# Kernel optimization log

Measured on AMD Instinct MI355X. Metric: run time of the kernel, lower is better.

The kernel has to match this reference:

```python
import jax, jax.numpy as jnp
import numpy as np

# GDN (gated delta-rule) linear attention, prefill path, single packed sequence,
# no initial conv/ssm state.
NUM_K_HEADS = 16
NUM_V_HEADS = 32
HEAD_K_DIM = 128
HEAD_V_DIM = 128
HIDDEN = 2048
CONV_K = 4
EPS = 1e-6
K_TOTAL = NUM_K_HEADS * HEAD_K_DIM
V_TOTAL = NUM_V_HEADS * HEAD_V_DIM
QKV_TOTAL = 2 * K_TOTAL + V_TOTAL


def setup_inputs() -> dict:
    key = jax.random.key(0)
    ks = jax.random.split(key, 9)
    T = 2048
    s = 0.02
    return {
        "hidden_states": jax.random.normal(ks[0], (T, HIDDEN), jnp.float32),
        "in_proj_qkv_weight": s * jax.random.normal(ks[1], (QKV_TOTAL, HIDDEN), jnp.float32),
        "in_proj_z_weight": s * jax.random.normal(ks[2], (V_TOTAL, HIDDEN), jnp.float32),
        "in_proj_a_weight": s * jax.random.normal(ks[3], (NUM_V_HEADS, HIDDEN), jnp.float32),
        "in_proj_b_weight": s * jax.random.normal(ks[4], (NUM_V_HEADS, HIDDEN), jnp.float32),
        "conv1d_weight": 0.1 * jax.random.normal(ks[5], (QKV_TOTAL, CONV_K), jnp.float32),
        "out_proj_weight": s * jax.random.normal(ks[6], (HIDDEN, V_TOTAL), jnp.float32),
        "norm_weight": jnp.ones((HEAD_V_DIM,), jnp.float32),
        "A_log": jnp.log(jnp.linspace(1.0, 8.0, NUM_V_HEADS, dtype=jnp.float32)),
        "dt_bias": 0.5 * jax.random.normal(ks[7], (NUM_V_HEADS,), jnp.float32),
    }


def _causal_conv1d_silu(x, w):
    # x: [T, C], w: [C, K] depthwise causal conv + SiLU
    T = x.shape[0]
    K = w.shape[1]
    xp = jnp.pad(x, ((K - 1, 0), (0, 0)))
    y = xp[0:T] * w[:, 0]
    for j in range(1, K):  # small fixed K
        y = y + xp[j:j + T] * w[:, j]
    return jax.nn.silu(y)


def _l2norm(x):
    return x / jnp.sqrt(jnp.sum(x * x, axis=-1, keepdims=True) + EPS)


def _gdn_recurrence(q, k, v, g, beta, scale):
    # q,k: [T,Hv,Dk] (l2-normed, repeated over GQA groups), v: [T,Hv,Dv]
    # g,beta: [T,Hv]. State S: [Hv,Dk,Dv]. Gated delta rule:
    #   S <- exp(g)*S ; S <- S + k^T beta (v - k S) ; o = scale * q S
    Hv, Dk = q.shape[1], q.shape[2]
    Dv = v.shape[2]

    def step(S, inp):
        q_t, k_t, v_t, g_t, b_t = inp
        S = S * jnp.exp(g_t)[:, None, None]
        pred = jnp.einsum('hk,hkv->hv', k_t, S)
        delta = b_t[:, None] * (v_t - pred)
        S = S + jnp.einsum('hk,hv->hkv', k_t, delta)
        o = jnp.einsum('hk,hkv->hv', q_t * scale, S)
        return S, o

    S0 = jnp.zeros((Hv, Dk, Dv), q.dtype)
    _, o = jax.lax.scan(step, S0, (q, k, v, g, beta))
    return o  # [T,Hv,Dv]


def reference(hidden_states, in_proj_qkv_weight, in_proj_z_weight, in_proj_a_weight,
              in_proj_b_weight, conv1d_weight, out_proj_weight, norm_weight, A_log, dt_bias):
    T = hidden_states.shape[0]
    mixed = hidden_states @ in_proj_qkv_weight.T            # [T, QKV_TOTAL]
    z = hidden_states @ in_proj_z_weight.T                  # [T, V_TOTAL]
    a = hidden_states @ in_proj_a_weight.T                  # [T, Hv]
    b = hidden_states @ in_proj_b_weight.T                  # [T, Hv]

    mixed = _causal_conv1d_silu(mixed, conv1d_weight)

    q, k, v = jnp.split(mixed, [K_TOTAL, 2 * K_TOTAL], axis=-1)
    q = q.reshape(T, NUM_K_HEADS, HEAD_K_DIM)
    k = k.reshape(T, NUM_K_HEADS, HEAD_K_DIM)
    v = v.reshape(T, NUM_V_HEADS, HEAD_V_DIM)

    # qk l2-norm in kernel, GQA repeat to v heads
    q = _l2norm(q)
    k = _l2norm(k)
    ratio = NUM_V_HEADS // NUM_K_HEADS
    q = jnp.repeat(q, ratio, axis=1)
    k = jnp.repeat(k, ratio, axis=1)

    # fused_gdn_gating: g = -exp(A_log) * softplus(a + dt_bias); beta = sigmoid(b)
    g = -jnp.exp(A_log) * jax.nn.softplus(a + dt_bias)      # [T,Hv]
    beta = jax.nn.sigmoid(b)                                # [T,Hv]

    o = _gdn_recurrence(q, k, v, g, beta, HEAD_K_DIM ** -0.5)  # [T,Hv,Dv]

    # gated RMSNorm: rmsnorm(o) * norm_weight * silu(z)
    o = o * jax.lax.rsqrt(jnp.mean(o * o, axis=-1, keepdims=True) + EPS) * norm_weight
    o = o * jax.nn.silu(z.reshape(T, NUM_V_HEADS, HEAD_V_DIM))

    return o.reshape(T, -1) @ out_proj_weight.T             # [T, HIDDEN]
```

## Files before the change

### kernel.cpp

```cpp
#include <hip/hip_runtime.h>
#include <math.h>

#define T_SEQ     2048
#define HIDDEN_D  2048
#define NUM_KH    16
#define NUM_VH    32
#define HEAD_DIM  128
#define K_TOTAL   2048
#define V_TOTAL   4096
#define QKV_TOTAL 8192
#define EPS_F     1e-6f
#define CC        32
#define NCHUNK    (T_SEQ / CC)
#define NV        8

typedef __attribute__((ext_vector_type(4))) float f32x4;
typedef __attribute__((ext_vector_type(8))) short s16x8;

__device__ __forceinline__ unsigned short f2bf(float f) {
    unsigned int u = __float_as_uint(f);
    u += 0x7FFFu + ((u >> 16) & 1u);
    return (unsigned short)(u >> 16);
}

__device__ __forceinline__ float bf2f(unsigned short h) {
    return __uint_as_float((unsigned int)h << 16);
}

__global__ __launch_bounds__(256) void cast_bf16_kernel(
    const float* __restrict__ src, unsigned short* __restrict__ dst, int n4)
{
    int idx = blockIdx.x * 256 + threadIdx.x;
    if (idx >= n4) return;
    float4 v = ((const float4*)src)[idx];
    ushort4 o;
    o.x = f2bf(v.x); o.y = f2bf(v.y); o.z = f2bf(v.z); o.w = f2bf(v.w);
    ((ushort4*)dst)[idx] = o;
}

__global__ __launch_bounds__(256) void gemm_bt_bf16(
    const unsigned short* __restrict__ A, const unsigned short* __restrict__ B,
    float* __restrict__ C, int M, int N, int K)
{
    __shared__ unsigned short As[128 * 64];
    __shared__ unsigned short Bs[128 * 64];
    const int tid  = threadIdx.x;
    const int wave = tid >> 6;
    const int lane = tid & 63;
    const int m0 = blockIdx.y * 128;
    const int n0 = blockIdx.x * 128;
    const int wm = (wave >> 1) * 64;
    const int wn = (wave & 1) * 64;

    f32x4 acc[4][4];
    f32x4 zero = {0.f, 0.f, 0.f, 0.f};
#pragma unroll
    for (int i = 0; i < 4; ++i)
#pragma unroll
        for (int j = 0; j < 4; ++j) acc[i][j] = zero;

    const int srow = lane >> 3;
    const int scol = (lane & 7) * 8;
    const int rm = lane & 15;
    const int koq = (lane >> 4) * 8;

    for (int kt = 0; kt < K; kt += 64) {
#pragma unroll
        for (int l = 0; l < 4; ++l) {
            const int r0 = wave * 32 + l * 8;
            const unsigned short* ga =
                A + (size_t)(m0 + r0 + srow) * K + kt + scol;
            const unsigned short* gb =
                B + (size_t)(n0 + r0 + srow) * K + kt + scol;
            __builtin_amdgcn_global_load_lds(
                (const __attribute__((address_space(1))) void*)ga,
                (__attribute__((address_space(3))) void*)&As[r0 * 64], 16, 0, 0);
            __builtin_amdgcn_global_load_lds(
                (const __attribute__((address_space(1))) void*)gb,
                (__attribute__((address_space(3))) void*)&Bs[r0 * 64], 16, 0, 0);
        }
        __syncthreads();

#pragma unroll
        for (int ks = 0; ks < 2; ++ks) {
            const int ko = ks * 32 + koq;
            s16x8 af[4], bfr[4];
#pragma unroll
            for (int i = 0; i < 4; ++i) {
                af[i]  = *(const s16x8*)&As[(wm + i * 16 + rm) * 64 + ko];
                bfr[i] = *(const s16x8*)&Bs[(wn + i * 16 + rm) * 64 + ko];
            }
#pragma unroll
            for (int i = 0; i < 4; ++i)
#pragma unroll
                for (int j = 0; j < 4; ++j)
                    acc[i][j] = __builtin_amdgcn_mfma_f32_16x16x32_bf16(
                        af[i], bfr[j], acc[i][j], 0, 0, 0);
        }
        __syncthreads();
    }

    const int cr = (lane >> 4) * 4;
    const int ccol = lane & 15;
#pragma unroll
    for (int i = 0; i < 4; ++i)
#pragma unroll
        for (int j = 0; j < 4; ++j) {
#pragma unroll
            for (int r = 0; r < 4; ++r)
                C[(size_t)(m0 + wm + i * 16 + cr + r) * N
                  + n0 + wn + j * 16 + ccol] = acc[i][j][r];
        }
}

__global__ __launch_bounds__(256) void gemm_nt_64(
    const float* __restrict__ A, const float* __restrict__ B,
    float* __restrict__ C, int M, int N, int K)
{
    __shared__ float As[16][68];
    __shared__ float Bs[16][68];
    const int tid = threadIdx.x;
    const int m0 = blockIdx.y * 64;
    const int n0 = blockIdx.x * 64;
    const int tm = tid >> 4;
    const int tn = tid & 15;
    const int lr = tid >> 2;
    const int lc = (tid & 3) * 4;

    float acc[4][4];
#pragma unroll
    for (int i = 0; i < 4; ++i)
#pragma unroll
        for (int j = 0; j < 4; ++j) acc[i][j] = 0.f;

    for (int kt = 0; kt < K; kt += 16) {
        float4 av = *(const float4*)(A + (size_t)(m0 + lr) * K + kt + lc);
        float4 bv = *(const float4*)(B + (size_t)(n0 + lr) * K + kt + lc);
        As[lc + 0][lr] = av.x; As[lc + 1][lr] = av.y;
        As[lc + 2][lr] = av.z; As[lc + 3][lr] = av.w;
        Bs[lc + 0][lr] = bv.x; Bs[lc + 1][lr] = bv.y;
        Bs[lc + 2][lr] = bv.z; Bs[lc + 3][lr] = bv.w;
        __syncthreads();
#pragma unroll
        for (int kk = 0; kk < 16; ++kk) {
            float4 a4 = *(const float4*)&As[kk][tm * 4];
            float4 b4 = *(const float4*)&Bs[kk][tn * 4];
            float a[4] = {a4.x, a4.y, a4.z, a4.w};
            float b[4] = {b4.x, b4.y, b4.z, b4.w};
#pragma unroll
            for (int i = 0; i < 4; ++i)
#pragma unroll
                for (int j = 0; j < 4; ++j)
                    acc[i][j] = fmaf(a[i], b[j], acc[i][j]);
        }
        __syncthreads();
    }
#pragma unroll
    for (int i = 0; i < 4; ++i) {
        float4 o = make_float4(acc[i][0], acc[i][1], acc[i][2], acc[i][3]);
        *(float4*)(C + (size_t)(m0 + tm * 4 + i) * N + n0 + tn * 4) = o;
    }
}

__global__ __launch_bounds__(256) void concat_ab_kernel(
    const float* __restrict__ Wa, const float* __restrict__ Wb,
    float* __restrict__ Wab)
{
    int idx = blockIdx.x * 256 + threadIdx.x;
    int half = 16384;
    const float* src = (idx < half) ? Wa : Wb;
    int off = (idx < half) ? idx : idx - half;
    ((float4*)Wab)[idx] = ((const float4*)src)[off];
}

__global__ __launch_bounds__(256) void gating_finalize_kernel(
    const float* __restrict__ ab, const float* __restrict__ A_log,
    const float* __restrict__ dt_bias, float* __restrict__ g,
    float* __restrict__ beta)
{
    int idx = blockIdx.x * 256 + threadIdx.x;
    int t = idx >> 5, h = idx & 31;
    float a = ab[t * 64 + h] + dt_bias[h];
    float b = ab[t * 64 + 32 + h];
    float sp = (a > 20.f) ? a : log1pf(expf(a));
    g[idx] = -expf(A_log[h]) * sp;
    beta[idx] = 1.f / (1.f + expf(-b));
}

__global__ __launch_bounds__(256) void conv_silu_kernel(
    const float* __restrict__ mixed, const float* __restrict__ cw,
    float* __restrict__ qkv)
{
    int idx = blockIdx.x * 256 + threadIdx.x;
    int c = idx & (QKV_TOTAL - 1);
    int t = idx >> 13;
    const float4 w = *(const float4*)(cw + (size_t)c * 4);
    float y = w.w * mixed[(size_t)t * QKV_TOTAL + c];
    if (t >= 1) y = fmaf(w.z, mixed[(size_t)(t - 1) * QKV_TOTAL + c], y);
    if (t >= 2) y = fmaf(w.y, mixed[(size_t)(t - 2) * QKV_TOTAL + c], y);
    if (t >= 3) y = fmaf(w.x, mixed[(size_t)(t - 3) * QKV_TOTAL + c], y);
    qkv[(size_t)t * QKV_TOTAL + c] = y / (1.f + expf(-y));
}

__global__ __launch_bounds__(64) void l2norm_kernel(float* __restrict__ qkv)
{
    const int row = blockIdx.x;
    const int t = row >> 5;
    const int r = row & 31;
    float* p = qkv + (size_t)t * QKV_TOTAL + r * HEAD_DIM;
    const int lane = threadIdx.x;
    float2 v = *(float2*)(p + lane * 2);
    float s = v.x * v.x + v.y * v.y;
    for (int off = 32; off > 0; off >>= 1) s += __shfl_down(s, off);
    s = __shfl(s, 0);
    float inv = rsqrtf(s + EPS_F);
    v.x *= inv; v.y *= inv;
    *(float2*)(p + lane * 2) = v;
}

__global__ __launch_bounds__(256) void gdn_p1(
    const float* __restrict__ qkv, const float* __restrict__ g,
    const float* __restrict__ beta, float* __restrict__ PTbuf,
    unsigned short* __restrict__ K2buf, float* __restrict__ lam_g,
    float* __restrict__ bet_g)
{
    __shared__ float Kn[CC][132];
    __shared__ float Qn[CC][132];
    __shared__ float Wm[CC][33];
    __shared__ float Tld[CC][36];
    __shared__ float Pm[CC][33];
    __shared__ float Trl[CC][33];
    __shared__ float cums[CC];
    __shared__ float betas[CC];
    __shared__ float rlS[CC];

    const int tid = threadIdx.x;
    const int h   = blockIdx.x;
    const int cix = blockIdx.y;
    const int t0  = cix * CC;
    const int kh  = h >> 1;
    const float scale = 0.08838834764831845f;
    const size_t mb = ((size_t)cix * NUM_VH + h);
    const size_t sb = mb * CC;

    if (tid < CC) {
        float x = g[(size_t)(t0 + tid) * NUM_VH + h];
        float bv = beta[(size_t)(t0 + tid) * NUM_VH + h];
#pragma unroll
        for (int off = 1; off < 32; off <<= 1) {
            float n = __shfl_up(x, off);
            if (tid >= off) x += n;
        }
        cums[tid] = x;
        betas[tid] = bv;
        float c31 = __shfl(x, 31);
        lam_g[sb + tid] = expf(x);
        bet_g[sb + tid] = bv;
        rlS[tid] = expf(c31 - x);
    }
#pragma unroll
    for (int p = 0; p < 4; ++p) {
        int idx = p * 256 + tid;
        int i = idx >> 5, k4 = (idx & 31) * 4;
        const float* qr = qkv + (size_t)(t0 + i) * QKV_TOTAL + kh * HEAD_DIM + k4;
        float4 q4 = *(const float4*)qr;
        float4 k4v = *(const float4*)(qr + K_TOTAL);
        *(float4*)&Kn[i][k4] = k4v;
        q4.x *= scale; q4.y *= scale; q4.z *= scale; q4.w *= scale;
        *(float4*)&Qn[i][k4] = q4;
    }
    __syncthreads();

    {
        const int i0 = (tid >> 4) * 2, j0 = (tid & 15) * 2;
        float wa[2][2] = {{0.f, 0.f}, {0.f, 0.f}};
        float pa[2][2] = {{0.f, 0.f}, {0.f, 0.f}};
        for (int k = 0; k < HEAD_DIM; k += 4) {
            float4 a0 = *(const float4*)&Kn[i0][k];
            float4 a1 = *(const float4*)&Kn[i0 + 1][k];
            float4 b0 = *(const float4*)&Kn[j0][k];
            float4 b1 = *(const float4*)&Kn[j0 + 1][k];
            float4 c0 = *(const float4*)&Qn[i0][k];
            float4 c1 = *(const float4*)&Qn[i0 + 1][k];
            const float* ap0 = (const float*)&a0;
            const float* ap1 = (const float*)&a1;
            const float* bp0 = (const float*)&b0;
            const float* bp1 = (const float*)&b1;
            const float* cp0 = (const float*)&c0;
            const float* cp1 = (const float*)&c1;
#pragma unroll
            for (int cc = 0; cc < 4; ++cc) {
                wa[0][0] = fmaf(ap0[cc], bp0[cc], wa[0][0]);
                wa[0][1] = fmaf(ap0[cc], bp1[cc], wa[0][1]);
                wa[1][0] = fmaf(ap1[cc], bp0[cc], wa[1][0]);
                wa[1][1] = fmaf(ap1[cc], bp1[cc], wa[1][1]);
                pa[0][0] = fmaf(cp0[cc], bp0[cc], pa[0][0]);
                pa[0][1] = fmaf(cp0[cc], bp1[cc], pa[0][1]);
                pa[1][0] = fmaf(cp1[cc], bp0[cc], pa[1][0]);
                pa[1][1] = fmaf(cp1[cc], bp1[cc], pa[1][1]);
            }
        }
#pragma unroll
        for (int di = 0; di < 2; ++di)
#pragma unroll
            for (int dj = 0; dj < 2; ++dj) {
                int i = i0 + di, j = j0 + dj;
                float rr = expf(fminf(cums[i] - cums[j], 0.f));
                Wm[i][j] = (j < i) ? betas[i] * rr * wa[di][dj] : 0.f;
                Pm[i][j] = (j <= i) ? rr * pa[di][dj] : 0.f;
            }
    }
    __syncthreads();

    {
        const int col = tid >> 3, tk = tid & 7;
        if (tk == 0) Tld[0][col] = (col == 0) ? 1.f : 0.f;
        for (int i = 1; i < CC; ++i) {
            float part = 0.f;
            for (int j = tk; j < i; j += 8)
                part = fmaf(Wm[i][j], Tld[j][col], part);
            part += __shfl_xor(part, 4);
            part += __shfl_xor(part, 2);
            part += __shfl_xor(part, 1);
            if (tk == 0) Tld[i][col] = ((i == col) ? 1.f : 0.f) - part;
        }
    }
    __syncthreads();

    {
        const int i = tid >> 3, j0 = (tid & 7) * 4;
        const float r = rlS[i];
#pragma unroll
        for (int e = 0; e < 4; ++e)
            Trl[i][j0 + e] = Tld[i][j0 + e] * r;
        float4 accp = {0.f, 0.f, 0.f, 0.f};
        for (int m = 0; m < CC; ++m) {
            float pv = Pm[i][m];
            float4 tv = *(const float4*)&Tld[m][j0];
            accp.x = fmaf(pv, tv.x, accp.x);
            accp.y = fmaf(pv, tv.y, accp.y);
            accp.z = fmaf(pv, tv.z, accp.z);
            accp.w = fmaf(pv, tv.w, accp.w);
        }
        *(float4*)(PTbuf + mb * (CC * CC) + tid * 4) = accp;
    }
    __syncthreads();

    {
        const int m0 = tid >> 3;
        const int q  = (tid & 7) * 4;
        float acc[4][4];
#pragma unroll
        for (int c = 0; c < 4; ++c)
#pragma unroll
            for (int e = 0; e < 4; ++e) acc[c][e] = 0.f;
        for (int j = 0; j < CC; ++j) {
            float t = Trl[j][m0];
#pragma unroll
            for (int c = 0; c < 4; ++c) {
                float4 a = *(const float4*)&Kn[j][q + 32 * c];
                acc[c][0] = fmaf(t, a.x, acc[c][0]);
                acc[c][1] = fmaf(t, a.y, acc[c][1]);
                acc[c][2] = fmaf(t, a.z, acc[c][2]);
                acc[c][3] = fmaf(t, a.w, acc[c][3]);
            }
        }
        unsigned short* kout =
            K2buf + mb * (CC * HEAD_DIM) + m0 * HEAD_DIM + q;
#pragma unroll
        for (int c = 0; c < 4; ++c) {
            ushort4 o4;
            o4.x = f2bf(acc[c][0]); o4.y = f2bf(acc[c][1]);
            o4.z = f2bf(acc[c][2]); o4.w = f2bf(acc[c][3]);
            *(ushort4*)(kout + 32 * c) = o4;
        }
    }
}

__global__ __launch_bounds__(256) void gdn_p2(
    const float* __restrict__ qkv, const float* __restrict__ PTbuf,
    const unsigned short* __restrict__ K2buf, const float* __restrict__ lam_g,
    const float* __restrict__ bet_g, float* __restrict__ o)
{
    __shared__ float Kn[CC][128];
    __shared__ float Qn[CC][128];
    __shared__ unsigned short K2l[2][CC][128];
    __shared__ float PTl[2][CC][36];
    __shared__ float Sm[HEAD_DIM][NV + 2];
    __shared__ float Dl[CC][NV + 2];
    __shared__ float lamS[2][CC], betS[2][CC];

    const int tid = threadIdx.x;
    const int wv  = tid >> 6;
    const int ln  = tid & 63;
    const int h   = blockIdx.x >> 4;
    const int V0  = (blockIdx.x & 15) * NV;
    const int kh  = h >> 1;
    const float scale = 0.08838834764831845f;

    const int ri = tid >> 3;
    const int rn = (tid & 3) * 2;
    const int hh = (tid >> 2) & 1;
    const int hh4 = hh * 4;
    const int rx = ri & 3;

    const int fk = (tid >> 3) * 4;
    const int sn = tid & 7;

    const int drow = wv * 2 + (ln >> 5);
    const int dw   = ln & 31;

#define DMA_KQ(T0)                                                            \
    {                                                                         \
        _Pragma("unroll")                                                     \
        for (int p = 0; p < 4; ++p) {                                         \
            const int i = p * 8 + drow;                                       \
            const int u = dw ^ ((i & 3) << 1);                                \
            const float* sq = qkv + (size_t)((T0) + i) * QKV_TOTAL            \
                              + kh * HEAD_DIM + u * 4;                        \
            __builtin_amdgcn_global_load_lds(                                 \
                (const __attribute__((address_space(1))) void*)(sq + K_TOTAL),\
                (__attribute__((address_space(3))) void*)                     \
                    &Kn[p * 8 + wv * 2][0], 16, 0, 0);                        \
            __builtin_amdgcn_global_load_lds(                                 \
                (const __attribute__((address_space(1))) void*)sq,            \
                (__attribute__((address_space(3))) void*)                     \
                    &Qn[p * 8 + wv * 2][0], 16, 0, 0);                        \
        }                                                                     \
    }

#define DMA_K2(MB, BUF)                                                       \
    {                                                                         \
        _Pragma("unroll")                                                     \
        for (int p = 0; p < 2; ++p) {                                         \
            const unsigned short* sk = K2buf + (MB) * (CC * HEAD_DIM)         \
                                       + p * 2048 + wv * 512 + ln * 8;        \
            __builtin_amdgcn_global_load_lds(                                 \
                (const __attribute__((address_space(1))) void*)sk,            \
                (__attribute__((address_space(3))) void*)                     \
                    &K2l[BUF][p * 16 + wv * 4][0], 16, 0, 0);                 \
        }                                                                     \
    }

#pragma unroll
    for (int c = 0; c < 4; ++c) Sm[fk + c][sn] = 0.f;

    DMA_KQ(0);
    DMA_K2((size_t)h, 0);
    {
        float4 pt0 = *(const float4*)(PTbuf + (size_t)h * (CC * CC) + tid * 4);
        *(float4*)&PTl[0][tid >> 3][(tid & 7) * 4] = pt0;
        if (tid < CC) {
            lamS[0][tid] = lam_g[(size_t)h * CC + tid];
            betS[0][tid] = bet_g[(size_t)h * CC + tid];
        }
    }
    float2 vR = *(const float2*)(qkv + (size_t)ri * QKV_TOTAL
                                 + 2 * K_TOTAL + h * HEAD_DIM + V0 + rn);

    int cur = 0;
    for (int cix = 0; cix < NCHUNK; ++cix) {
        const int t0 = cix * CC;
        __syncthreads();

        const float lam = lamS[cur][ri];
        const float bet = betS[cur][ri];
        float r1x = 0.f, r1y = 0.f, r2x = 0.f, r2y = 0.f;
#pragma unroll
        for (int kk = 0; kk < 16; ++kk) {
            const int cp = ((kk ^ rx) << 3) + hh4;
            const int cl = (kk << 3) + hh4;
            float4 kv = *(const float4*)&Kn[ri][cp];
            float4 qv = *(const float4*)&Qn[ri][cp];
            const float* kp = (const float*)&kv;
            const float* qp = (const float*)&qv;
#pragma unroll
            for (int c4 = 0; c4 < 4; ++c4) {
                float2 s = *(const float2*)&Sm[cl + c4][rn];
                r1x = fmaf(kp[c4], s.x, r1x);
                r1y = fmaf(kp[c4], s.y, r1y);
                r2x = fmaf(qp[c4], s.x, r2x);
                r2y = fmaf(qp[c4], s.y, r2y);
            }
        }
        r1x += __shfl_xor(r1x, 4);
        r1y += __shfl_xor(r1y, 4);
        r2x += __shfl_xor(r2x, 4);
        r2y += __shfl_xor(r2y, 4);
        {
            float dlx = bet * (vR.x - lam * r1x);
            float dly = bet * (vR.y - lam * r1y);
            if (hh == 0) { Dl[ri][rn] = dlx; Dl[ri][rn + 1] = dly; }
        }
        const float lsc = lam * scale;
        float ox = r2x * lsc, oy = r2y * lsc;
        __syncthreads();

        const int nxt = cur ^ 1;
        float4 ptN; float lamN = 0.f, betN = 0.f; float2 vN;
        const int more = (cix + 1 < NCHUNK);
        if (more) {
            const int t0n = t0 + CC;
            const size_t mbn = (size_t)(cix + 1) * NUM_VH + h;
            DMA_KQ(t0n);
            DMA_K2(mbn, nxt);
            ptN = *(const float4*)(PTbuf + mbn * (CC * CC) + tid * 4);
            if (tid < CC) {
                lamN = lam_g[mbn * CC + tid];
                betN = bet_g[mbn * CC + tid];
            }
            vN = *(const float2*)(qkv + (size_t)(t0n + ri) * QKV_TOTAL
                                  + 2 * K_TOTAL + h * HEAD_DIM + V0 + rn);
        }

        {
            for (int j = 0; j < CC; ++j) {
                float p = PTl[cur][ri][j];
                float2 d = *(const float2*)&Dl[j][rn];
                ox = fmaf(p, d.x, ox);
                oy = fmaf(p, d.y, oy);
            }
            if (hh == 0)
                *(float2*)(o + (size_t)(t0 + ri) * V_TOTAL + h * HEAD_DIM + V0 + rn)
                    = make_float2(ox, oy);
        }

        {
            const float lamL = lamS[cur][CC - 1];
            float s0 = lamL * Sm[fk + 0][sn];
            float s1 = lamL * Sm[fk + 1][sn];
            float s2 = lamL * Sm[fk + 2][sn];
            float s3 = lamL * Sm[fk + 3][sn];
            for (int j = 0; j < CC; ++j) {
                ushort4 kk = *(const ushort4*)&K2l[cur][j][fk];
                float d = Dl[j][sn];
                s0 = fmaf(bf2f(kk.x), d, s0);
                s1 = fmaf(bf2f(kk.y), d, s1);
                s2 = fmaf(bf2f(kk.z), d, s2);
                s3 = fmaf(bf2f(kk.w), d, s3);
            }
            Sm[fk + 0][sn] = s0;
            Sm[fk + 1][sn] = s1;
            Sm[fk + 2][sn] = s2;
            Sm[fk + 3][sn] = s3;
        }

        if (more) {
            *(float4*)&PTl[nxt][tid >> 3][(tid & 7) * 4] = ptN;
            if (tid < CC) { lamS[nxt][tid] = lamN; betS[nxt][tid] = betN; }
            vR = vN;
        }
        cur = nxt;
    }
#undef DMA_KQ
#undef DMA_K2
}

__global__ __launch_bounds__(64) void rmsnorm_gate_kernel(
    float* __restrict__ o, const float* __restrict__ z,
    const float* __restrict__ nw)
{
    const int row = blockIdx.x;
    float* p = o + (size_t)row * HEAD_DIM;
    const float* zp = z + (size_t)row * HEAD_DIM;
    const int lane = threadIdx.x;
    float2 v = *(float2*)(p + lane * 2);
    float s = v.x * v.x + v.y * v.y;
    for (int off = 32; off > 0; off >>= 1) s += __shfl_down(s, off);
    s = __shfl(s, 0);
    float inv = rsqrtf(s * (1.f / HEAD_DIM) + EPS_F);
    float2 zv = *(float2*)(zp + lane * 2);
    float2 wv = *(const float2*)(nw + lane * 2);
    v.x = v.x * inv * wv.x * (zv.x / (1.f + expf(-zv.x)));
    v.y = v.y * inv * wv.y * (zv.y / (1.f + expf(-zv.y)));
    *(float2*)(p + lane * 2) = v;
}

extern "C" void kernel_launch(void* const* d_in, const int* in_sizes, int n_in,
                              void* d_out, int out_size, void* d_ws,
                              size_t ws_size, hipStream_t stream)
{
    const float* hs    = (const float*)d_in[0];
    const float* Wqkv  = (const float*)d_in[1];
    const float* Wz    = (const float*)d_in[2];
    const float* Wa    = (const float*)d_in[3];
    const float* Wb    = (const float*)d_in[4];
    const float* cw    = (const float*)d_in[5];
    const float* Wout  = (const float*)d_in[6];
    const float* nw    = (const float*)d_in[7];
    const float* A_log = (const float*)d_in[8];
    const float* dtb   = (const float*)d_in[9];
    float* out = (float*)d_out;

    float* F     = (float*)d_ws;
    float* mixed = F;
    float* qkvb  = F + (size_t)16777216;
    float* zb    = F + (size_t)33554432;
    float* gb    = F + (size_t)41943040;
    float* bb    = F + (size_t)42008576;
    float* ob    = mixed;

    float* PTbuf = F + (size_t)8388608;
    unsigned short* K2buf = (unsigned short*)(F + (size_t)10485760);
    float* lam_b = F + (size_t)14680064;
    float* bet_b = F + (size_t)14745600;

    unsigned short* hs_bf   = (unsigned short*)(F + (size_t)16777216);
    unsigned short* Wqkv_bf = (unsigned short*)(F + (size_t)18874368);
    unsigned short* Wz_bf   = (unsigned short*)(F + (size_t)27262976);
    unsigned short* ob_bf   = (unsigned short*)(F + (size_t)33554432);
    unsigned short* Wout_bf = (unsigned short*)(F + (size_t)37748736);

    float* Wab = F + (size_t)27262976;
    float* ab  = F + (size_t)27394048;

    cast_bf16_kernel<<<1048576 / 256, 256, 0, stream>>>(hs, hs_bf, 1048576);
    cast_bf16_kernel<<<4194304 / 256, 256, 0, stream>>>(Wqkv, Wqkv_bf, 4194304);
    cast_bf16_kernel<<<2097152 / 256, 256, 0, stream>>>(Wz, Wz_bf, 2097152);
    gemm_bt_bf16<<<dim3(QKV_TOTAL / 128, T_SEQ / 128), 256, 0, stream>>>(
        hs_bf, Wqkv_bf, mixed, T_SEQ, QKV_TOTAL, HIDDEN_D);
    gemm_bt_bf16<<<dim3(V_TOTAL / 128, T_SEQ / 128), 256, 0, stream>>>(
        hs_bf, Wz_bf, zb, T_SEQ, V_TOTAL, HIDDEN_D);
    concat_ab_kernel<<<32768 / 256, 256, 0, stream>>>(Wa, Wb, Wab);
    gemm_nt_64<<<dim3(1, T_SEQ / 64), 256, 0, stream>>>(
        hs, Wab, ab, T_SEQ, 64, HIDDEN_D);
    gating_finalize_kernel<<<(T_SEQ * NUM_VH) / 256, 256, 0, stream>>>(
        ab, A_log, dtb, gb, bb);
    conv_silu_kernel<<<(T_SEQ * QKV_TOTAL) / 256, 256, 0, stream>>>(
        mixed, cw, qkvb);
    l2norm_kernel<<<T_SEQ * 32, 64, 0, stream>>>(qkvb);
    gdn_p1<<<dim3(NUM_VH, NCHUNK), 256, 0, stream>>>(
        qkvb, gb, bb, PTbuf, K2buf, lam_b, bet_b);
    gdn_p2<<<NUM_VH * (HEAD_DIM / NV), 256, 0, stream>>>(
        qkvb, PTbuf, K2buf, lam_b, bet_b, ob);
    rmsnorm_gate_kernel<<<T_SEQ * NUM_VH, 64, 0, stream>>>(ob, zb, nw);
    cast_bf16_kernel<<<2097152 / 256, 256, 0, stream>>>(ob, ob_bf, 2097152);
    cast_bf16_kernel<<<2097152 / 256, 256, 0, stream>>>(Wout, Wout_bf, 2097152);
    gemm_bt_bf16<<<dim3(HIDDEN_D / 128, T_SEQ / 128), 256, 0, stream>>>(
        ob_bf, Wout_bf, out, T_SEQ, HIDDEN_D, V_TOTAL);
}
```

Measured before the change: 1.056 ms.

## Fuse qk conv with l2norm into bf16 buffer and store PT in bf16

Splits the conv+SiLU into a v-only fp32 kernel and a q/k kernel that also does the L2 normalisation and writes bf16, removing the separate l2norm pass and an fp32 round trip. gdn_p1 and gdn_p2 now read q/k as bf16, PTbuf is stored as bf16, and gdn_p2 keeps q/k in LDS as bf16 with a new swizzle and launch bounds set to 2 blocks per CU. This cuts memory traffic and LDS footprint in the recurrence at the cost of reduced precision for q, k and the PT matrices, plus a rearranged workspace layout.

```diff
diff --git a/kernel.cpp b/kernel.cpp
--- a/kernel.cpp
+++ b/kernel.cpp
@@ -16,6 +16,7 @@
 
 typedef __attribute__((ext_vector_type(4))) float f32x4;
 typedef __attribute__((ext_vector_type(8))) short s16x8;
+typedef __attribute__((ext_vector_type(8))) unsigned short u16x8;
 
 __device__ __forceinline__ unsigned short f2bf(float f) {
     unsigned int u = __float_as_uint(f);
@@ -187,40 +188,63 @@
     beta[idx] = 1.f / (1.f + expf(-b));
 }
 
-__global__ __launch_bounds__(256) void conv_silu_kernel(
+__global__ __launch_bounds__(256) void conv_v_kernel(
     const float* __restrict__ mixed, const float* __restrict__ cw,
-    float* __restrict__ qkv)
+    float* __restrict__ vb)
 {
     int idx = blockIdx.x * 256 + threadIdx.x;
-    int c = idx & (QKV_TOTAL - 1);
-    int t = idx >> 13;
-    const float4 w = *(const float4*)(cw + (size_t)c * 4);
-    float y = w.w * mixed[(size_t)t * QKV_TOTAL + c];
-    if (t >= 1) y = fmaf(w.z, mixed[(size_t)(t - 1) * QKV_TOTAL + c], y);
-    if (t >= 2) y = fmaf(w.y, mixed[(size_t)(t - 2) * QKV_TOTAL + c], y);
-    if (t >= 3) y = fmaf(w.x, mixed[(size_t)(t - 3) * QKV_TOTAL + c], y);
-    qkv[(size_t)t * QKV_TOTAL + c] = y / (1.f + expf(-y));
-}
-
-__global__ __launch_bounds__(64) void l2norm_kernel(float* __restrict__ qkv)
+    int c = idx & (V_TOTAL - 1);
+    int t = idx >> 12;
+    int ch = 2 * K_TOTAL + c;
+    const float4 w = *(const float4*)(cw + (size_t)ch * 4);
+    const float* base = mixed + (size_t)t * QKV_TOTAL + ch;
+    float y = w.w * base[0];
+    if (t >= 1) y = fmaf(w.z, base[-QKV_TOTAL], y);
+    if (t >= 2) y = fmaf(w.y, base[-2 * QKV_TOTAL], y);
+    if (t >= 3) y = fmaf(w.x, base[-3 * QKV_TOTAL], y);
+    vb[idx] = y / (1.f + expf(-y));
+}
+
+__global__ __launch_bounds__(64) void convqk_l2_kernel(
+    const float* __restrict__ mixed, const float* __restrict__ cw,
+    unsigned short* __restrict__ qk_bf)
 {
     const int row = blockIdx.x;
     const int t = row >> 5;
     const int r = row & 31;
-    float* p = qkv + (size_t)t * QKV_TOTAL + r * HEAD_DIM;
     const int lane = threadIdx.x;
-    float2 v = *(float2*)(p + lane * 2);
-    float s = v.x * v.x + v.y * v.y;
+    const int c = r * HEAD_DIM + lane * 2;
+    const float4 w0 = *(const float4*)(cw + (size_t)c * 4);
+    const float4 w1 = *(const float4*)(cw + (size_t)(c + 1) * 4);
+    const float* base = mixed + (size_t)t * QKV_TOTAL + c;
+    float2 x0 = *(const float2*)base;
+    float y0 = w0.w * x0.x, y1 = w1.w * x0.y;
+    if (t >= 1) {
+        float2 x = *(const float2*)(base - QKV_TOTAL);
+        y0 = fmaf(w0.z, x.x, y0); y1 = fmaf(w1.z, x.y, y1);
+    }
+    if (t >= 2) {
+        float2 x = *(const float2*)(base - 2 * QKV_TOTAL);
+        y0 = fmaf(w0.y, x.x, y0); y1 = fmaf(w1.y, x.y, y1);
+    }
+    if (t >= 3) {
+        float2 x = *(const float2*)(base - 3 * QKV_TOTAL);
+        y0 = fmaf(w0.x, x.x, y0); y1 = fmaf(w1.x, x.y, y1);
+    }
+    y0 = y0 / (1.f + expf(-y0));
+    y1 = y1 / (1.f + expf(-y1));
+    float s = y0 * y0 + y1 * y1;
     for (int off = 32; off > 0; off >>= 1) s += __shfl_down(s, off);
     s = __shfl(s, 0);
     float inv = rsqrtf(s + EPS_F);
-    v.x *= inv; v.y *= inv;
-    *(float2*)(p + lane * 2) = v;
+    unsigned short* qb = qk_bf + (size_t)t * 4096 + c;
+    qb[0] = f2bf(y0 * inv);
+    qb[1] = f2bf(y1 * inv);
 }
 
 __global__ __launch_bounds__(256) void gdn_p1(
-    const float* __restrict__ qkv, const float* __restrict__ g,
-    const float* __restrict__ beta, float* __restrict__ PTbuf,
+    const unsigned short* __restrict__ qk_bf, const float* __restrict__ g,
+    const float* __restrict__ beta, unsigned short* __restrict__ PTbuf,
     unsigned short* __restrict__ K2buf, float* __restrict__ lam_g,
     float* __restrict__ bet_g)
 {
@@ -259,15 +283,26 @@
         rlS[tid] = expf(c31 - x);
     }
 #pragma unroll
-    for (int p = 0; p < 4; ++p) {
+    for (int p = 0; p < 2; ++p) {
         int idx = p * 256 + tid;
-        int i = idx >> 5, k4 = (idx & 31) * 4;
-        const float* qr = qkv + (size_t)(t0 + i) * QKV_TOTAL + kh * HEAD_DIM + k4;
-        float4 q4 = *(const float4*)qr;
-        float4 k4v = *(const float4*)(qr + K_TOTAL);
-        *(float4*)&Kn[i][k4] = k4v;
-        q4.x *= scale; q4.y *= scale; q4.z *= scale; q4.w *= scale;
-        *(float4*)&Qn[i][k4] = q4;
+        int i = idx >> 4, ch = (idx & 15) * 8;
+        const unsigned short* qr =
+            qk_bf + (size_t)(t0 + i) * 4096 + kh * HEAD_DIM + ch;
+        u16x8 q8 = *(const u16x8*)qr;
+        u16x8 k8 = *(const u16x8*)(qr + K_TOTAL);
+        float4 kf0, kf1, qf0, qf1;
+        kf0.x = bf2f(k8[0]); kf0.y = bf2f(k8[1]);
+        kf0.z = bf2f(k8[2]); kf0.w = bf2f(k8[3]);
+        kf1.x = bf2f(k8[4]); kf1.y = bf2f(k8[5]);
+        kf1.z = bf2f(k8[6]); kf1.w = bf2f(k8[7]);
+        qf0.x = bf2f(q8[0]) * scale; qf0.y = bf2f(q8[1]) * scale;
+        qf0.z = bf2f(q8[2]) * scale; qf0.w = bf2f(q8[3]) * scale;
+        qf1.x = bf2f(q8[4]) * scale; qf1.y = bf2f(q8[5]) * scale;
+        qf1.z = bf2f(q8[6]) * scale; qf1.w = bf2f(q8[7]) * scale;
+        *(float4*)&Kn[i][ch]     = kf0;
+        *(float4*)&Kn[i][ch + 4] = kf1;
+        *(float4*)&Qn[i][ch]     = qf0;
+        *(float4*)&Qn[i][ch + 4] = qf1;
     }
     __syncthreads();
 
@@ -342,7 +377,10 @@
             accp.z = fmaf(pv, tv.z, accp.z);
             accp.w = fmaf(pv, tv.w, accp.w);
         }
-        *(float4*)(PTbuf + mb * (CC * CC) + tid * 4) = accp;
+        ushort4 pt4;
+        pt4.x = f2bf(accp.x); pt4.y = f2bf(accp.y);
+        pt4.z = f2bf(accp.z); pt4.w = f2bf(accp.w);
+        *(ushort4*)(PTbuf + mb * (CC * CC) + tid * 4) = pt4;
     }
     __syncthreads();
 
@@ -377,13 +415,14 @@
     }
 }
 
-__global__ __launch_bounds__(256) void gdn_p2(
-    const float* __restrict__ qkv, const float* __restrict__ PTbuf,
+__global__ __launch_bounds__(256, 2) void gdn_p2(
+    const float* __restrict__ vb, const unsigned short* __restrict__ qk_bf,
+    const unsigned short* __restrict__ PTbuf,
     const unsigned short* __restrict__ K2buf, const float* __restrict__ lam_g,
     const float* __restrict__ bet_g, float* __restrict__ o)
 {
-    __shared__ float Kn[CC][128];
-    __shared__ float Qn[CC][128];
+    __shared__ unsigned short Kn[CC][128];
+    __shared__ unsigned short Qn[CC][128];
     __shared__ unsigned short K2l[2][CC][128];
     __shared__ float PTl[2][CC][36];
     __shared__ float Sm[HEAD_DIM][NV + 2];
@@ -401,31 +440,30 @@
     const int ri = tid >> 3;
     const int rn = (tid & 3) * 2;
     const int hh = (tid >> 2) & 1;
-    const int hh4 = hh * 4;
-    const int rx = ri & 3;
+    const int rx2 = ri & 3;
 
     const int fk = (tid >> 3) * 4;
     const int sn = tid & 7;
 
-    const int drow = wv * 2 + (ln >> 5);
-    const int dw   = ln & 31;
+    const int drow = ln >> 4;
+    const int dc   = ln & 15;
 
 #define DMA_KQ(T0)                                                            \
     {                                                                         \
         _Pragma("unroll")                                                     \
-        for (int p = 0; p < 4; ++p) {                                         \
-            const int i = p * 8 + drow;                                       \
-            const int u = dw ^ ((i & 3) << 1);                                \
-            const float* sq = qkv + (size_t)((T0) + i) * QKV_TOTAL            \
-                              + kh * HEAD_DIM + u * 4;                        \
+        for (int p = 0; p < 2; ++p) {                                         \
+            const int i = p * 16 + wv * 4 + drow;                             \
+            const int sc = 2 * ((dc >> 1) ^ (i & 3)) + (dc & 1);              \
+            const unsigned short* sq = qk_bf + (size_t)((T0) + i) * 4096      \
+                                       + kh * HEAD_DIM + sc * 8;              \
             __builtin_amdgcn_global_load_lds(                                 \
                 (const __attribute__((address_space(1))) void*)(sq + K_TOTAL),\
                 (__attribute__((address_space(3))) void*)                     \
-                    &Kn[p * 8 + wv * 2][0], 16, 0, 0);                        \
+                    &Kn[p * 16 + wv * 4][0], 16, 0, 0);                       \
             __builtin_amdgcn_global_load_lds(                                 \
                 (const __attribute__((address_space(1))) void*)sq,            \
                 (__attribute__((address_space(3))) void*)                     \
-                    &Qn[p * 8 + wv * 2][0], 16, 0, 0);                        \
+                    &Qn[p * 16 + wv * 4][0], 16, 0, 0);                       \
         }                                                                     \
     }
 
@@ -448,15 +486,18 @@
     DMA_KQ(0);
     DMA_K2((size_t)h, 0);
     {
-        float4 pt0 = *(const float4*)(PTbuf + (size_t)h * (CC * CC) + tid * 4);
-        *(float4*)&PTl[0][tid >> 3][(tid & 7) * 4] = pt0;
+        ushort4 pt0 = *(const ushort4*)(PTbuf + (size_t)h * (CC * CC) + tid * 4);
+        float4 pf;
+        pf.x = bf2f(pt0.x); pf.y = bf2f(pt0.y);
+        pf.z = bf2f(pt0.z); pf.w = bf2f(pt0.w);
+        *(float4*)&PTl[0][tid >> 3][(tid & 7) * 4] = pf;
         if (tid < CC) {
             lamS[0][tid] = lam_g[(size_t)h * CC + tid];
             betS[0][tid] = bet_g[(size_t)h * CC + tid];
         }
     }
-    float2 vR = *(const float2*)(qkv + (size_t)ri * QKV_TOTAL
-                                 + 2 * K_TOTAL + h * HEAD_DIM + V0 + rn);
+    float2 vR = *(const float2*)(vb + (size_t)ri * V_TOTAL
+                                 + h * HEAD_DIM + V0 + rn);
 
     int cur = 0;
     for (int cix = 0; cix < NCHUNK; ++cix) {
@@ -467,20 +508,20 @@
         const float bet = betS[cur][ri];
         float r1x = 0.f, r1y = 0.f, r2x = 0.f, r2y = 0.f;
 #pragma unroll
-        for (int kk = 0; kk < 16; ++kk) {
-            const int cp = ((kk ^ rx) << 3) + hh4;
-            const int cl = (kk << 3) + hh4;
-            float4 kv = *(const float4*)&Kn[ri][cp];
-            float4 qv = *(const float4*)&Qn[ri][cp];
-            const float* kp = (const float*)&kv;
-            const float* qp = (const float*)&qv;
-#pragma unroll
-            for (int c4 = 0; c4 < 4; ++c4) {
-                float2 s = *(const float2*)&Sm[cl + c4][rn];
-                r1x = fmaf(kp[c4], s.x, r1x);
-                r1y = fmaf(kp[c4], s.y, r1y);
-                r2x = fmaf(qp[c4], s.x, r2x);
-                r2y = fmaf(qp[c4], s.y, r2y);
+        for (int kk = 0; kk < 8; ++kk) {
+            const int pc = (2 * (kk ^ rx2) + hh) * 8;
+            const int cl = kk * 16 + hh * 8;
+            u16x8 kv = *(const u16x8*)&Kn[ri][pc];
+            u16x8 qv = *(const u16x8*)&Qn[ri][pc];
+#pragma unroll
+            for (int c8 = 0; c8 < 8; ++c8) {
+                float kf = bf2f(kv[c8]);
+                float qf = bf2f(qv[c8]);
+                float2 s = *(const float2*)&Sm[cl + c8][rn];
+                r1x = fmaf(kf, s.x, r1x);
+                r1y = fmaf(kf, s.y, r1y);
+                r2x = fmaf(qf, s.x, r2x);
+                r2y = fmaf(qf, s.y, r2y);
             }
         }
         r1x += __shfl_xor(r1x, 4);
@@ -497,20 +538,20 @@
         __syncthreads();
 
         const int nxt = cur ^ 1;
-        float4 ptN; float lamN = 0.f, betN = 0.f; float2 vN;
+        ushort4 ptN; float lamN = 0.f, betN = 0.f; float2 vN;
         const int more = (cix + 1 < NCHUNK);
         if (more) {
             const int t0n = t0 + CC;
             const size_t mbn = (size_t)(cix + 1) * NUM_VH + h;
             DMA_KQ(t0n);
             DMA_K2(mbn, nxt);
-            ptN = *(const float4*)(PTbuf + mbn * (CC * CC) + tid * 4);
+            ptN = *(const ushort4*)(PTbuf + mbn * (CC * CC) + tid * 4);
             if (tid < CC) {
                 lamN = lam_g[mbn * CC + tid];
                 betN = bet_g[mbn * CC + tid];
             }
-            vN = *(const float2*)(qkv + (size_t)(t0n + ri) * QKV_TOTAL
-                                  + 2 * K_TOTAL + h * HEAD_DIM + V0 + rn);
+            vN = *(const float2*)(vb + (size_t)(t0n + ri) * V_TOTAL
+                                  + h * HEAD_DIM + V0 + rn);
         }
 
         {
@@ -546,7 +587,10 @@
         }
 
         if (more) {
-            *(float4*)&PTl[nxt][tid >> 3][(tid & 7) * 4] = ptN;
+            float4 pf;
+            pf.x = bf2f(ptN.x); pf.y = bf2f(ptN.y);
+            pf.z = bf2f(ptN.z); pf.w = bf2f(ptN.w);
+            *(float4*)&PTl[nxt][tid >> 3][(tid & 7) * 4] = pf;
             if (tid < CC) { lamS[nxt][tid] = lamN; betS[nxt][tid] = betN; }
             vR = vN;
         }
@@ -594,25 +638,23 @@
 
     float* F     = (float*)d_ws;
     float* mixed = F;
-    float* qkvb  = F + (size_t)16777216;
-    float* zb    = F + (size_t)33554432;
-    float* gb    = F + (size_t)41943040;
-    float* bb    = F + (size_t)42008576;
-    float* ob    = mixed;
-
-    float* PTbuf = F + (size_t)8388608;
-    unsigned short* K2buf = (unsigned short*)(F + (size_t)10485760);
-    float* lam_b = F + (size_t)14680064;
-    float* bet_b = F + (size_t)14745600;
-
+    float* ob    = F;
+    unsigned short* PTbuf = (unsigned short*)(F + (size_t)8388608);
+    unsigned short* K2buf = (unsigned short*)(F + (size_t)9437184);
+    float* lam_b = F + (size_t)13631488;
+    float* bet_b = F + (size_t)13697024;
     unsigned short* hs_bf   = (unsigned short*)(F + (size_t)16777216);
     unsigned short* Wqkv_bf = (unsigned short*)(F + (size_t)18874368);
+    float* vb = F + (size_t)16777216;
+    unsigned short* qk_bf = (unsigned short*)(F + (size_t)25165824);
     unsigned short* Wz_bf   = (unsigned short*)(F + (size_t)27262976);
+    float* Wab = F + (size_t)27262976;
+    float* ab  = F + (size_t)27394048;
+    float* zb  = F + (size_t)33554432;
     unsigned short* ob_bf   = (unsigned short*)(F + (size_t)33554432);
     unsigned short* Wout_bf = (unsigned short*)(F + (size_t)37748736);
-
-    float* Wab = F + (size_t)27262976;
-    float* ab  = F + (size_t)27394048;
+    float* gb = F + (size_t)41943040;
+    float* bb = F + (size_t)42008576;
 
     cast_bf16_kernel<<<1048576 / 256, 256, 0, stream>>>(hs, hs_bf, 1048576);
     cast_bf16_kernel<<<4194304 / 256, 256, 0, stream>>>(Wqkv, Wqkv_bf, 4194304);
@@ -626,13 +668,13 @@
         hs, Wab, ab, T_SEQ, 64, HIDDEN_D);
     gating_finalize_kernel<<<(T_SEQ * NUM_VH) / 256, 256, 0, stream>>>(
         ab, A_log, dtb, gb, bb);
-    conv_silu_kernel<<<(T_SEQ * QKV_TOTAL) / 256, 256, 0, stream>>>(
-        mixed, cw, qkvb);
-    l2norm_kernel<<<T_SEQ * 32, 64, 0, stream>>>(qkvb);
+    conv_v_kernel<<<(T_SEQ * V_TOTAL) / 256, 256, 0, stream>>>(
+        mixed, cw, vb);
+    convqk_l2_kernel<<<T_SEQ * 32, 64, 0, stream>>>(mixed, cw, qk_bf);
     gdn_p1<<<dim3(NUM_VH, NCHUNK), 256, 0, stream>>>(
-        qkvb, gb, bb, PTbuf, K2buf, lam_b, bet_b);
+        qk_bf, gb, bb, PTbuf, K2buf, lam_b, bet_b);
     gdn_p2<<<NUM_VH * (HEAD_DIM / NV), 256, 0, stream>>>(
-        qkvb, PTbuf, K2buf, lam_b, bet_b, ob);
+        vb, qk_bf, PTbuf, K2buf, lam_b, bet_b, ob);
     rmsnorm_gate_kernel<<<T_SEQ * NUM_VH, 64, 0, stream>>>(ob, zb, nw);
     cast_bf16_kernel<<<2097152 / 256, 256, 0, stream>>>(ob, ob_bf, 2097152);
     cast_bf16_kernel<<<2097152 / 256, 256, 0, stream>>>(Wout, Wout_bf, 2097152);
```

After: 929.4 us. 12.0% less time.
